# Optimization experiments

Measured on AMD Instinct MI355X. Metric: run time of the kernel, lower is better.

Reference implementation:

```python
import jax, jax.numpy as jnp
import numpy as np

B, N = 16, 4096
CH = 64          # channel
S = 1024         # groups (FPS samples)
K = 32           # kneighbors
D = 2 * CH       # aggregation width (in == out, residual-safe)
EPS_STD = 1e-5
BN_EPS = 1e-5
SLOPE = 0.01


def setup_inputs() -> dict:
    key = jax.random.key(0)
    ks = jax.random.split(key, 8)
    return {
        "xyz": jax.random.normal(ks[0], (B, N, 3), jnp.float32),
        "points": jax.random.normal(ks[1], (B, N, CH), jnp.float32),
        # LocalGrouper affine (use_xyz=False -> width CH)
        "affine_alpha": jnp.ones((1, 1, 1, CH), jnp.float32),
        "affine_beta": jnp.zeros((1, 1, 1, CH), jnp.float32),
        # Local_Aggregation: conv1d(k=1) + BN, twice
        "w1": jax.random.normal(ks[2], (D, D), jnp.float32) / np.sqrt(D),
        "b1": jax.random.normal(ks[3], (D,), jnp.float32) * 0.01,
        "g1": jnp.ones((D,), jnp.float32),
        "be1": jnp.zeros((D,), jnp.float32),
        "w2": jax.random.normal(ks[4], (D, D), jnp.float32) / np.sqrt(D),
        "b2": jax.random.normal(ks[5], (D,), jnp.float32) * 0.01,
        "g2": jnp.ones((D,), jnp.float32),
        "be2": jnp.zeros((D,), jnp.float32),
    }


def _fps_single(xyz):
    # Furthest point sampling for one cloud [N,3] -> [S] int32 (starts at index 0, matching CUDA FPS)
    n = xyz.shape[0]

    def body(carry, _):
        min_d, last = carry
        d = jnp.sum((xyz - xyz[last]) ** 2, axis=-1)   # [N]
        min_d = jnp.minimum(min_d, d)
        nxt = jnp.argmax(min_d).astype(jnp.int32)
        return (min_d, nxt), nxt

    init = (jnp.full((n,), 1e10, xyz.dtype), jnp.int32(0))
    _, idx_rest = jax.lax.scan(body, init, None, length=S - 1)
    return jnp.concatenate([jnp.zeros((1,), jnp.int32), idx_rest])


def _knn_single(xyz, new_xyz):
    # squared dists [S,N]; K smallest via top_k on negated distances
    d = (jnp.sum(new_xyz ** 2, -1, keepdims=True)
         + jnp.sum(xyz ** 2, -1)[None, :]
         - 2.0 * new_xyz @ xyz.T)
    _, idx = jax.lax.top_k(-d, K)
    return idx  # [S,K]


def _bn(x, g, b):
    # BatchNorm1d in training mode: batch stats over (batch, length) dims of [M, C, K]
    m = jnp.mean(x, axis=(0, 2), keepdims=True)
    v = jnp.mean((x - m) ** 2, axis=(0, 2), keepdims=True)  # biased var, as torch BN
    return g[None, :, None] * (x - m) * jax.lax.rsqrt(v + BN_EPS) + b[None, :, None]


def reference(xyz, points, affine_alpha, affine_beta, w1, b1, g1, be1, w2, b2, g2, be2):
    # ---- LocalGrouper ----
    fps_idx = jax.vmap(_fps_single)(xyz)                              # [B,S]
    new_xyz = jnp.take_along_axis(xyz, fps_idx[..., None], axis=1)    # [B,S,3]
    new_pts = jnp.take_along_axis(points, fps_idx[..., None], axis=1) # [B,S,CH]
    idx = jax.vmap(_knn_single)(xyz, new_xyz)                         # [B,S,K]
    grouped = jax.vmap(lambda p, i: p[i])(points, idx)                # [B,S,K,CH]

    # normalize == 'center': mean over neighbors, std over whole per-batch tensor (unbiased, as torch.std)
    mean = jnp.mean(grouped, axis=2, keepdims=True)                   # [B,S,1,CH]
    diff = grouped - mean
    cnt = S * K * CH
    var = jnp.sum(diff.reshape(B, -1) ** 2, axis=-1) / (cnt - 1)      # [B]
    std = jnp.sqrt(var)[:, None, None, None]                          # [B,1,1,1]
    grouped = affine_alpha * (diff / (std + EPS_STD)) + affine_beta

    new_feature = jnp.concatenate(
        [grouped, jnp.broadcast_to(new_pts[:, :, None, :], (B, S, K, CH))], axis=-1
    )                                                                  # [B,S,K,2*CH]

    # ---- Local_Aggregation ----
    x = new_feature.transpose(0, 1, 3, 2).reshape(B * S, D, K)         # [BS, D, K]
    h = jnp.einsum('oc,mck->mok', w1, x) + b1[None, :, None]
    h = jax.nn.leaky_relu(_bn(h, g1, be1), SLOPE)
    h = jnp.einsum('oc,mck->mok', w2, h) + b2[None, :, None]
    h = jax.nn.leaky_relu(_bn(h, g2, be2) + x, SLOPE)
    pooled = jnp.max(h, axis=-1).reshape(B, S, D)                      # adaptive_max_pool1d(.,1)
    return (new_xyz, pooled)
```

## Files before the change

kernel.cpp:

```cpp
#include <hip/hip_runtime.h>

#define DI __device__ __forceinline__

typedef __attribute__((ext_vector_type(8))) short v8s;
typedef __attribute__((ext_vector_type(4))) short v4s;
typedef __attribute__((ext_vector_type(4))) float v4f;
typedef unsigned long long u64;

constexpr int BB = 16, NN = 4096, CH = 64, SS = 1024, KK = 32, DD = 128;
constexpr int LDW = 136;
constexpr int GPC = 2;
constexpr int GGRID = 512;

constexpr size_t OFF_FPSIDX = 0;
constexpr size_t OFF_KNN    = 65536;
constexpr size_t OFF_MEAN   = 2162688;
constexpr size_t OFF_VARB   = 6356992;
constexpr size_t OFF_BINS1  = 6361088;
constexpr size_t OFF_BINS2  = 6426624;
constexpr size_t OFF_RSTD   = 6492160;
constexpr size_t OFF_COEF1  = 6492224;
constexpr size_t OFF_COEF2  = 6493248;
constexpr size_t OFF_W1BF   = 6494272;
constexpr size_t OFF_W2BF   = 6527040;
constexpr size_t OFF_XYZT   = 6559808;
constexpr size_t MEMSET_OFF = OFF_VARB;
constexpr size_t MEMSET_LEN = 4096 + 65536 + 65536;

DI short f2bf(float f) {
  unsigned u = __float_as_uint(f);
  u = (u + 0x7fffu + ((u >> 16) & 1u)) >> 16;
  return (short)u;
}
DI float bf2f(short s) { return __uint_as_float(((unsigned)(unsigned short)s) << 16); }

__global__ void prep_kernel(const float* __restrict__ xyz, float* __restrict__ xyzT,
                            const float* __restrict__ w1, const float* __restrict__ w2,
                            short* __restrict__ w1b, short* __restrict__ w2b) {
  int bid = blockIdx.x;
  if (bid < 256) {
    int i = bid * 256 + threadIdx.x;
    int b = i >> 12, n = i & 4095;
    const float* s = xyz + (size_t)i * 3;
    float* d = xyzT + (size_t)b * 3 * NN + n;
    d[0] = s[0]; d[NN] = s[1]; d[2 * NN] = s[2];
  } else {
    int i = (bid - 256) * 256 + threadIdx.x;
    w1b[i] = f2bf(w1[i]);
    w2b[i] = f2bf(w2[i]);
  }
}

DI double tag12(double d, int tag) {
  u64 b = (u64)__double_as_longlong(d);
  b = (b & ~0xFFFull) | (u64)(unsigned)tag;
  return __longlong_as_double((long long)b);
}
template <int CTRL>
DI double dpp_fmax64(double x) {
  u64 b = (u64)__double_as_longlong(x);
  int lo = __builtin_amdgcn_update_dpp(0, (int)(unsigned)b, CTRL, 0xf, 0xf, true);
  int hi = __builtin_amdgcn_update_dpp(0, (int)(unsigned)(b >> 32), CTRL, 0xf, 0xf, true);
  double o = __longlong_as_double((long long)(((u64)(unsigned)hi << 32) | (unsigned)lo));
  return fmax(x, o);
}
DI double readlane_f64(double x, int l) {
  u64 b = (u64)__double_as_longlong(x);
  unsigned lo = (unsigned)__builtin_amdgcn_readlane((int)(unsigned)b, l);
  unsigned hi = (unsigned)__builtin_amdgcn_readlane((int)(unsigned)(b >> 32), l);
  return __longlong_as_double((long long)(((u64)hi << 32) | lo));
}

template <int N>
DI float dpp_ror_f(float v) {
  return __int_as_float(__builtin_amdgcn_update_dpp(0, __float_as_int(v), 0x120 + N, 0xf, 0xf, true));
}
DI float sum16(float v) {
  v += dpp_ror_f<1>(v);
  v += dpp_ror_f<2>(v);
  v += dpp_ror_f<4>(v);
  v += dpp_ror_f<8>(v);
  return v;
}
DI float max16(float v) {
  v = fmaxf(v, dpp_ror_f<1>(v));
  v = fmaxf(v, dpp_ror_f<2>(v));
  v = fmaxf(v, dpp_ror_f<4>(v));
  v = fmaxf(v, dpp_ror_f<8>(v));
  return v;
}

__global__ __launch_bounds__(512, 2) void fps_kernel(const float* __restrict__ xyzT,
                                                     int* __restrict__ fps_idx,
                                                     float* __restrict__ out_xyz) {
  int b = blockIdx.x, tid = threadIdx.x;
  int wave = tid >> 6, lane = tid & 63;
  const float* bx = xyzT + (size_t)b * 3 * NN;
  const float* by = bx + NN;
  const float* bz = bx + 2 * NN;
  __shared__ float4 s_xyzw[NN];
  __shared__ int s_fidx[SS];
  __shared__ double s_pd[2][8];

  double px64[8], py64[8], pz64[8], pp64[8], m64[8];
  int tagbase = 4095 - tid;
#pragma unroll
  for (int k = 0; k < 8; ++k) {
    int gi = k * 512 + tid;
    float x = bx[gi], y = by[gi], z = bz[gi];
    s_xyzw[gi] = make_float4(x, y, z, 0.f);
    px64[k] = (double)x; py64[k] = (double)y; pz64[k] = (double)z;
    pp64[k] = fma(px64[k], px64[k], fma(py64[k], py64[k], pz64[k] * pz64[k]));
    m64[k] = tag12(1e10, tagbase - k * 512);
  }
  if (tid == 0) s_fidx[0] = 0;
  __syncthreads();
  float4 c0 = s_xyzw[0];
  double cx = (double)c0.x, cy = (double)c0.y, cz = (double)c0.z;

  for (int j = 1; j < SS; ++j) {
    double cx2 = -2.0 * cx, cy2 = -2.0 * cy, cz2 = -2.0 * cz;
    double cc = fma(cx, cx, fma(cy, cy, cz * cz));
    double best;
#pragma unroll
    for (int k = 0; k < 8; ++k) {
      double d = fma(px64[k], cx2, fma(py64[k], cy2, fma(pz64[k], cz2, pp64[k] + cc)));
      d = fmax(d, 0.0);
      d = tag12(d, tagbase - k * 512);
      m64[k] = fmin(m64[k], d);
      best = (k == 0) ? m64[0] : fmax(best, m64[k]);
    }
    best = dpp_fmax64<0xB1>(best);
    best = dpp_fmax64<0x4E>(best);
    best = dpp_fmax64<0x141>(best);
    best = dpp_fmax64<0x140>(best);
    double r0 = readlane_f64(best, 0);
    double r1 = readlane_f64(best, 16);
    double r2 = readlane_f64(best, 32);
    double r3 = readlane_f64(best, 48);
    double bw = fmax(fmax(r0, r1), fmax(r2, r3));
    if (lane == 0) s_pd[j & 1][wave] = bw;
    __syncthreads();
    double bk = s_pd[j & 1][0];
#pragma unroll
    for (int w = 1; w < 8; ++w) bk = fmax(bk, s_pd[j & 1][w]);
    int fi = 4095 - (int)((u64)__double_as_longlong(bk) & 0xFFFull);
    float4 cw = s_xyzw[fi];
    cx = (double)cw.x; cy = (double)cw.y; cz = (double)cw.z;
    if (tid == 0) s_fidx[j] = fi;
  }
  __syncthreads();
  for (int t = tid; t < SS; t += 512) {
    int idx = s_fidx[t];
    fps_idx[b * SS + t] = idx;
    float4 p = s_xyzw[idx];
    out_xyz[((size_t)b * SS + t) * 3 + 0] = p.x;
    out_xyz[((size_t)b * SS + t) * 3 + 1] = p.y;
    out_xyz[((size_t)b * SS + t) * 3 + 2] = p.z;
  }
}

__global__ __launch_bounds__(256) void knn_kernel(const float* __restrict__ xyzT,
                                                  const int* __restrict__ fps_idx,
                                                  int* __restrict__ knn_idx) {
  int wave = threadIdx.x >> 6, lane = threadIdx.x & 63;
  int q = blockIdx.x * 4 + wave, b = q >> 10;
  const float* bx = xyzT + (size_t)b * 3 * NN;
  const float* by = bx + NN;
  const float* bz = bx + 2 * NN;
  int qi = fps_idx[q];
  float qx = bx[qi], qy = by[qi], qz = bz[qi];
  float d[64];
  float lmin = 1e30f;
#pragma unroll
  for (int j = 0; j < 64; ++j) {
    int n = j * 64 + lane;
    float dx = bx[n] - qx, dy = by[n] - qy, dz = bz[n] - qz;
    d[j] = fmaf(dx, dx, fmaf(dy, dy, dz * dz));
    lmin = fminf(lmin, d[j]);
  }
  unsigned lb = __float_as_uint(lmin);
  unsigned res = 0;
#pragma unroll
  for (int bit = 30; bit >= 0; --bit) {
    unsigned t = res | (1u << bit);
    int c = __popcll(__ballot(lb < t));
    res = (c < 32) ? t : res;
  }
  float tau = __uint_as_float(res) * 1.00001f + 1e-20f;

  __shared__ int ci[4][512];
  __shared__ u64 ck[4][512];
  int cnt = 0;
#pragma unroll
  for (int j = 0; j < 64; ++j) {
    bool pred = (d[j] <= tau);
    unsigned long long mask = __ballot(pred);
    if (pred) {
      int pos = cnt + __popcll(mask & ((1ull << lane) - 1ull));
      if (pos < 512) ci[wave][pos] = j * 64 + lane;
    }
    cnt += __popcll(mask);
  }
  if (cnt > 512) cnt = 512;
  double qx64 = (double)qx, qy64 = (double)qy, qz64 = (double)qz;
  for (int p = lane; p < cnt; p += 64) {
    int n = ci[wave][p];
    double dx = (double)bx[n] - qx64;
    double dy = (double)by[n] - qy64;
    double dz = (double)bz[n] - qz64;
    double d64 = fma(dx, dx, fma(dy, dy, dz * dz));
    ck[wave][p] = ((u64)__double_as_longlong(d64) & ~0xFFFull) | (u64)n;
  }
  for (int p = lane; p < cnt; p += 64) {
    u64 mykey = ck[wave][p];
    int rank = 0;
    int r = 0;
    for (; r + 4 <= cnt; r += 4) {
      u64 k0 = ck[wave][r + 0], k1 = ck[wave][r + 1];
      u64 k2 = ck[wave][r + 2], k3 = ck[wave][r + 3];
      rank += (k0 < mykey) + (k1 < mykey) + (k2 < mykey) + (k3 < mykey);
    }
    for (; r < cnt; ++r) rank += (ck[wave][r] < mykey) ? 1 : 0;
    if (rank < KK) knn_idx[(size_t)q * KK + rank] = (int)(mykey & 0xFFFull);
  }
}

__global__ __launch_bounds__(256) void meanvar_kernel(const float* __restrict__ points,
                                                      const int* __restrict__ kidx,
                                                      float* __restrict__ mean_out,
                                                      float* __restrict__ var_bins) {
  int wave = threadIdx.x >> 6, lane = threadIdx.x & 63;
  int xcd = blockIdx.x & 7, slot = blockIdx.x >> 3;
  int b = xcd + ((slot >> 8) << 3);
  int g = b * SS + (slot & 255) * 4 + wave;
  const float* pb = points + (size_t)b * NN * CH;
  const int* idx = kidx + (size_t)g * KK;
  float s1 = 0.f, s2 = 0.f;
#pragma unroll
  for (int k = 0; k < KK; ++k) {
    float x = pb[(size_t)idx[k] * CH + lane];
    s1 += x;
    s2 = fmaf(x, x, s2);
  }
  float m = s1 * (1.0f / 32.0f);
  mean_out[(size_t)g * CH + lane] = m;
  float part = s2 - s1 * m;
#pragma unroll
  for (int mm = 1; mm < 64; mm <<= 1) part += __shfl_xor(part, mm, 64);
  if (lane == 0) atomicAdd(&var_bins[b * 64 + (g & 63)], part);
}

__global__ void fin_std_kernel(const float* __restrict__ bins, float* __restrict__ rstd) {
  int t = threadIdx.x;
  if (t < BB) {
    float s = 0.f;
    for (int i = 0; i < 64; ++i) s += bins[t * 64 + i];
    float var = s / (float)(SS * KK * CH - 1);
    rstd[t] = 1.0f / (sqrtf(var) + 1e-5f);
  }
}

__global__ void fin_bn_kernel(const float* __restrict__ bins, const float* __restrict__ g,
                              const float* __restrict__ be, float* __restrict__ coef) {
  int o = threadIdx.x;
  float s = 0.f, qq = 0.f;
  for (int bin = 0; bin < 64; ++bin) {
    s += bins[(bin * 128 + o) * 2 + 0];
    qq += bins[(bin * 128 + o) * 2 + 1];
  }
  constexpr float invM = 1.0f / (float)(BB * SS * KK);
  float mean = s * invM;
  float var = qq * invM - mean * mean;
  if (var < 0.f) var = 0.f;
  float sc = g[o] / sqrtf(var + 1e-5f);
  coef[2 * o] = sc;
  coef[2 * o + 1] = be[o] - mean * sc;
}

template <int PASS>
__global__ __launch_bounds__(256, 2) void gemm_pass(
    const float* __restrict__ points, const int* __restrict__ kidx, const int* __restrict__ fidx,
    const float* __restrict__ mean, const float* __restrict__ rstd,
    const float* __restrict__ alpha, const float* __restrict__ beta,
    const short* __restrict__ w1bf, const short* __restrict__ w2bf,
    const float* __restrict__ coef1, const float* __restrict__ coef2,
    float* __restrict__ bins_out, float* __restrict__ out_pooled) {
  __shared__ short Xs[GPC * 32 * LDW];
  __shared__ short Ps[(PASS >= 1) ? (GPC * 32 * LDW) : 8];
  __shared__ float sMean[2][GPC][64];
  __shared__ float sAlpha[64], sBeta[64];
  __shared__ float sCoef1[256], sCoef2[256];
  __shared__ float bnS[128], bnQ[128];

  int tid = threadIdx.x;
  int wave = tid >> 6, lane = tid & 63;
  int q4 = lane >> 4, l15 = lane & 15;
  int ohalf = wave & 1, gsel = wave >> 1;

  v8s wf1[4][4];
  v8s wf2[4][4];
#pragma unroll
  for (int ot = 0; ot < 4; ++ot) {
    int row = ohalf * 64 + ot * 16 + l15;
#pragma unroll
    for (int cs = 0; cs < 4; ++cs) {
      wf1[ot][cs] = *(const v8s*)(w1bf + row * 128 + cs * 32 + q4 * 8);
      if constexpr (PASS >= 1) wf2[ot][cs] = *(const v8s*)(w2bf + row * 128 + cs * 32 + q4 * 8);
    }
  }
  if (tid < 64) { sAlpha[tid] = alpha[tid]; sBeta[tid] = beta[tid]; }
  if constexpr (PASS >= 1) sCoef1[tid] = coef1[tid];
  if constexpr (PASS == 2) sCoef2[tid] = coef2[tid];
  if constexpr (PASS <= 1) {
    if (tid < 128) { bnS[tid] = 0.f; bnQ[tid] = 0.f; }
  }

  int xcd = blockIdx.x & 7, slot = blockIdx.x >> 3;
  int sg = tid >> 7, sk = (tid >> 2) & 31, qr = tid & 3;
  int ch0 = (qr & 1) * 32;
  bool norm = (qr < 2);
  float rsA = rstd[xcd], rsB = rstd[xcd + 8];

  float svA[4][4] = {}, sqA[4][4] = {};

  float4 ldv[8];
  {
    int t = slot;
    int batch = xcd + ((t >> 9) << 3);
    int g0 = batch * SS + (t & 511) * GPC;
    int ggl = g0 + sg;
    int row = norm ? kidx[(size_t)ggl * KK + sk] : fidx[ggl];
    const float* src = points + (size_t)batch * NN * CH + (size_t)row * CH + ch0;
#pragma unroll
    for (int u = 0; u < 8; ++u) ldv[u] = *(const float4*)(src + u * 4);
    if (tid < 32) {
      int sg2 = tid >> 4, off = (tid & 15) << 2;
      float4 mv = *(const float4*)(mean + (size_t)(g0 + sg2) * CH + off);
      *(float4*)&sMean[0][sg2][off] = mv;
    }
  }
  __syncthreads();

  for (int it = 0; it < 16; ++it) {
    int t = slot + it * 64;
    int batch = xcd + ((t >> 9) << 3);
    int g0 = batch * SS + (t & 511) * GPC;
    int tn = (it < 15) ? t + 64 : t;
    int batch_n = xcd + ((tn >> 9) << 3);
    int g0_n = batch_n * SS + (tn & 511) * GPC;
    int ggl_n = g0_n + sg;
    int row_n = norm ? kidx[(size_t)ggl_n * KK + sk] : fidx[ggl_n];

    {
      float rs = (t >> 9) ? rsB : rsA;
      v8s pack[4];
#pragma unroll
      for (int u = 0; u < 8; ++u) {
        float4 vv = ldv[u];
        if (norm) {
          float4 mv = *(const float4*)&sMean[it & 1][sg][ch0 + u * 4];
          float4 av = *(const float4*)&sAlpha[ch0 + u * 4];
          float4 bv = *(const float4*)&sBeta[ch0 + u * 4];
          vv.x = fmaf((vv.x - mv.x) * rs, av.x, bv.x);
          vv.y = fmaf((vv.y - mv.y) * rs, av.y, bv.y);
          vv.z = fmaf((vv.z - mv.z) * rs, av.z, bv.z);
          vv.w = fmaf((vv.w - mv.w) * rs, av.w, bv.w);
        }
        pack[u >> 1][(u & 1) * 4 + 0] = f2bf(vv.x);
        pack[u >> 1][(u & 1) * 4 + 1] = f2bf(vv.y);
        pack[u >> 1][(u & 1) * 4 + 2] = f2bf(vv.z);
        pack[u >> 1][(u & 1) * 4 + 3] = f2bf(vv.w);
      }
      short* dst = &Xs[(sg * 32 + sk) * LDW + qr * 32];
#pragma unroll
      for (int p2 = 0; p2 < 4; ++p2) *(v8s*)(dst + p2 * 8) = pack[p2];
    }
    __syncthreads();

    v4f acc[4][2] = {};
#pragma unroll
    for (int cs = 0; cs < 4; ++cs) {
      v8s bfr[2];
#pragma unroll
      for (int kt = 0; kt < 2; ++kt)
        bfr[kt] = *(const v8s*)&Xs[(gsel * 32 + kt * 16 + l15) * LDW + cs * 32 + q4 * 8];
#pragma unroll
      for (int ot = 0; ot < 4; ++ot)
#pragma unroll
        for (int kt = 0; kt < 2; ++kt)
          acc[ot][kt] = __builtin_amdgcn_mfma_f32_16x16x32_bf16(wf1[ot][cs], bfr[kt], acc[ot][kt], 0, 0, 0);
    }

    float4 mpre;
    {
      const float* src = points + (size_t)batch_n * NN * CH + (size_t)row_n * CH + ch0;
#pragma unroll
      for (int u = 0; u < 8; ++u) ldv[u] = *(const float4*)(src + u * 4);
      if (tid < 32) {
        int sg2 = tid >> 4, off = (tid & 15) << 2;
        mpre = *(const float4*)(mean + (size_t)(g0_n + sg2) * CH + off);
      }
    }

    if constexpr (PASS == 0) {
#pragma unroll
      for (int ot = 0; ot < 4; ++ot)
#pragma unroll
        for (int r = 0; r < 4; ++r) {
          float a0 = acc[ot][0][r], a1 = acc[ot][1][r];
          svA[ot][r] += a0 + a1;
          sqA[ot][r] = fmaf(a0, a0, fmaf(a1, a1, sqA[ot][r]));
        }
    } else {
#pragma unroll
      for (int ot = 0; ot < 4; ++ot) {
        int o0 = ohalf * 64 + ot * 16 + q4 * 4;
#pragma unroll
        for (int kt = 0; kt < 2; ++kt) {
          v4s pk;
#pragma unroll
          for (int r = 0; r < 4; ++r) {
            float h = fmaf(acc[ot][kt][r], sCoef1[2 * (o0 + r)], sCoef1[2 * (o0 + r) + 1]);
            h = (h >= 0.f) ? h : 0.01f * h;
            pk[r] = f2bf(h);
          }
          *(v4s*)&Ps[(gsel * 32 + kt * 16 + l15) * LDW + o0] = pk;
        }
      }
      __syncthreads();

      v4f acc2[4][2] = {};
#pragma unroll
      for (int cs = 0; cs < 4; ++cs) {
        v8s pfr[2];
#pragma unroll
        for (int kt = 0; kt < 2; ++kt)
          pfr[kt] = *(const v8s*)&Ps[(gsel * 32 + kt * 16 + l15) * LDW + cs * 32 + q4 * 8];
#pragma unroll
        for (int ot = 0; ot < 4; ++ot)
#pragma unroll
          for (int kt = 0; kt < 2; ++kt)
            acc2[ot][kt] = __builtin_amdgcn_mfma_f32_16x16x32_bf16(wf2[ot][cs], pfr[kt], acc2[ot][kt], 0, 0, 0);
      }

      if constexpr (PASS == 1) {
#pragma unroll
        for (int ot = 0; ot < 4; ++ot)
#pragma unroll
          for (int r = 0; r < 4; ++r) {
            float a0 = acc2[ot][0][r], a1 = acc2[ot][1][r];
            svA[ot][r] += a0 + a1;
            sqA[ot][r] = fmaf(a0, a0, fmaf(a1, a1, sqA[ot][r]));
          }
      } else {
#pragma unroll
        for (int ot = 0; ot < 4; ++ot) {
          int o0 = ohalf * 64 + ot * 16 + q4 * 4;
          float mx[4] = {-1e30f, -1e30f, -1e30f, -1e30f};
#pragma unroll
          for (int kt = 0; kt < 2; ++kt) {
            v4s xv = *(const v4s*)&Xs[(gsel * 32 + kt * 16 + l15) * LDW + o0];
#pragma unroll
            for (int r = 0; r < 4; ++r) {
              float h = fmaf(acc2[ot][kt][r], sCoef2[2 * (o0 + r)], sCoef2[2 * (o0 + r) + 1]);
              float val = h + bf2f(xv[r]);
              val = (val >= 0.f) ? val : 0.01f * val;
              mx[r] = fmaxf(mx[r], val);
            }
          }
#pragma unroll
          for (int r = 0; r < 4; ++r) mx[r] = max16(mx[r]);
          if (l15 == 0) {
            float4 o4;
            o4.x = mx[0]; o4.y = mx[1]; o4.z = mx[2]; o4.w = mx[3];
            *(float4*)(out_pooled + (size_t)(g0 + gsel) * DD + o0) = o4;
          }
        }
      }
    }
    if (tid < 32) *(float4*)&sMean[(it + 1) & 1][tid >> 4][(tid & 15) << 2] = mpre;
    __syncthreads();
  }

  if constexpr (PASS <= 1) {
#pragma unroll
    for (int ot = 0; ot < 4; ++ot)
#pragma unroll
      for (int r = 0; r < 4; ++r) {
        float sv = sum16(svA[ot][r]);
        float sq = sum16(sqA[ot][r]);
        if (l15 == 0) {
          int o0 = ohalf * 64 + ot * 16 + q4 * 4;
          atomicAdd(&bnS[o0 + r], sv);
          atomicAdd(&bnQ[o0 + r], sq);
        }
      }
    __syncthreads();
    if (tid < 128) {
      float* bb = bins_out + (((blockIdx.x & 63) * 128 + tid) << 1);
      atomicAdd(bb, bnS[tid]);
      atomicAdd(bb + 1, bnQ[tid]);
    }
  }
}

extern "C" void kernel_launch(void* const* d_in, const int* in_sizes, int n_in,
                              void* d_out, int out_size, void* d_ws, size_t ws_size,
                              hipStream_t stream) {
  const float* xyz    = (const float*)d_in[0];
  const float* points = (const float*)d_in[1];
  const float* alpha  = (const float*)d_in[2];
  const float* beta   = (const float*)d_in[3];
  const float* w1     = (const float*)d_in[4];
  const float* g1     = (const float*)d_in[6];
  const float* be1    = (const float*)d_in[7];
  const float* w2     = (const float*)d_in[8];
  const float* g2     = (const float*)d_in[10];
  const float* be2    = (const float*)d_in[11];
  float* out = (float*)d_out;

  char* w = (char*)d_ws;
  int* fps_i   = (int*)(w + OFF_FPSIDX);
  int* knn_i   = (int*)(w + OFF_KNN);
  float* meanp = (float*)(w + OFF_MEAN);
  float* varb  = (float*)(w + OFF_VARB);
  float* bins1 = (float*)(w + OFF_BINS1);
  float* bins2 = (float*)(w + OFF_BINS2);
  float* rstdp = (float*)(w + OFF_RSTD);
  float* coef1 = (float*)(w + OFF_COEF1);
  float* coef2 = (float*)(w + OFF_COEF2);
  short* w1b   = (short*)(w + OFF_W1BF);
  short* w2b   = (short*)(w + OFF_W2BF);
  float* xyzT  = (float*)(w + OFF_XYZT);

  hipMemsetAsync(w + MEMSET_OFF, 0, MEMSET_LEN, stream);
  prep_kernel<<<320, 256, 0, stream>>>(xyz, xyzT, w1, w2, w1b, w2b);
  fps_kernel<<<BB, 512, 0, stream>>>(xyzT, fps_i, out);
  knn_kernel<<<(BB * SS) / 4, 256, 0, stream>>>(xyzT, fps_i, knn_i);
  meanvar_kernel<<<(BB * SS) / 4, 256, 0, stream>>>(points, knn_i, meanp, varb);
  fin_std_kernel<<<1, 64, 0, stream>>>(varb, rstdp);
  gemm_pass<0><<<GGRID, 256, 0, stream>>>(points, knn_i, fps_i, meanp, rstdp, alpha, beta,
                                          w1b, w2b, coef1, coef2, bins1, nullptr);
  fin_bn_kernel<<<1, 128, 0, stream>>>(bins1, g1, be1, coef1);
  gemm_pass<1><<<GGRID, 256, 0, stream>>>(points, knn_i, fps_i, meanp, rstdp, alpha, beta,
                                          w1b, w2b, coef1, coef2, bins2, nullptr);
  fin_bn_kernel<<<1, 128, 0, stream>>>(bins2, g2, be2, coef2);
  gemm_pass<2><<<GGRID, 256, 0, stream>>>(points, knn_i, fps_i, meanp, rstdp, alpha, beta,
                                          w1b, w2b, coef1, coef2, nullptr, out + (size_t)BB * SS * 3);
}
```

Baseline: 1.055 ms.

## Shrink FPS block to 4 waves, fuse mean/var into KNN, use packed bf16 converts

The FPS kernel now runs 256 threads, each holding 16 points, so the per-iteration cross-wave reduction covers 4 waves instead of 8. The clamp to zero on distances is dropped. The mean/variance kernel is merged into the KNN kernel, reusing the selected neighbor indices from shared memory and removing one launch plus a global reread of the indices. The GEMM passes use a packed bf16 conversion builtin instead of manual rounding. The cost is more registers per FPS thread and less parallelism within the serial FPS loop. The ci array is also reused in place, which could be unsafe if other lanes still read candidate entries when the writes happen.

```diff
diff --git a/kernel.cpp b/kernel.cpp
--- a/kernel.cpp
+++ b/kernel.cpp
@@ -34,6 +34,16 @@
 }
 DI float bf2f(short s) { return __uint_as_float(((unsigned)(unsigned short)s) << 16); }
 
+DI unsigned pkbf(float a, float b) {
+#if __has_builtin(__builtin_amdgcn_cvt_pk_bf16_f32)
+  typedef __attribute__((ext_vector_type(2))) __bf16 bf2_t;
+  bf2_t r = __builtin_amdgcn_cvt_pk_bf16_f32(a, b);
+  return *(unsigned*)&r;
+#else
+  return (unsigned)(unsigned short)f2bf(a) | ((unsigned)(unsigned short)f2bf(b) << 16);
+#endif
+}
+
 __global__ void prep_kernel(const float* __restrict__ xyz, float* __restrict__ xyzT,
                             const float* __restrict__ w1, const float* __restrict__ w2,
                             short* __restrict__ w1b, short* __restrict__ w2b) {
@@ -90,7 +100,7 @@
   return v;
 }
 
-__global__ __launch_bounds__(512, 2) void fps_kernel(const float* __restrict__ xyzT,
+__global__ __launch_bounds__(256, 1) void fps_kernel(const float* __restrict__ xyzT,
                                                      int* __restrict__ fps_idx,
                                                      float* __restrict__ out_xyz) {
   int b = blockIdx.x, tid = threadIdx.x;
@@ -100,18 +110,18 @@
   const float* bz = bx + 2 * NN;
   __shared__ float4 s_xyzw[NN];
   __shared__ int s_fidx[SS];
-  __shared__ double s_pd[2][8];
-
-  double px64[8], py64[8], pz64[8], pp64[8], m64[8];
+  __shared__ double s_pd[2][4];
+
+  double px64[16], py64[16], pz64[16], pp64[16], m64[16];
   int tagbase = 4095 - tid;
 #pragma unroll
-  for (int k = 0; k < 8; ++k) {
-    int gi = k * 512 + tid;
+  for (int k = 0; k < 16; ++k) {
+    int gi = k * 256 + tid;
     float x = bx[gi], y = by[gi], z = bz[gi];
     s_xyzw[gi] = make_float4(x, y, z, 0.f);
     px64[k] = (double)x; py64[k] = (double)y; pz64[k] = (double)z;
     pp64[k] = fma(px64[k], px64[k], fma(py64[k], py64[k], pz64[k] * pz64[k]));
-    m64[k] = tag12(1e10, tagbase - k * 512);
+    m64[k] = tag12(1e10, tagbase - k * 256);
   }
   if (tid == 0) s_fidx[0] = 0;
   __syncthreads();
@@ -123,10 +133,9 @@
     double cc = fma(cx, cx, fma(cy, cy, cz * cz));
     double best;
 #pragma unroll
-    for (int k = 0; k < 8; ++k) {
+    for (int k = 0; k < 16; ++k) {
       double d = fma(px64[k], cx2, fma(py64[k], cy2, fma(pz64[k], cz2, pp64[k] + cc)));
-      d = fmax(d, 0.0);
-      d = tag12(d, tagbase - k * 512);
+      d = tag12(d, tagbase - k * 256);
       m64[k] = fmin(m64[k], d);
       best = (k == 0) ? m64[0] : fmax(best, m64[k]);
     }
@@ -141,16 +150,15 @@
     double bw = fmax(fmax(r0, r1), fmax(r2, r3));
     if (lane == 0) s_pd[j & 1][wave] = bw;
     __syncthreads();
-    double bk = s_pd[j & 1][0];
-#pragma unroll
-    for (int w = 1; w < 8; ++w) bk = fmax(bk, s_pd[j & 1][w]);
+    double bk = fmax(fmax(s_pd[j & 1][0], s_pd[j & 1][1]),
+                     fmax(s_pd[j & 1][2], s_pd[j & 1][3]));
     int fi = 4095 - (int)((u64)__double_as_longlong(bk) & 0xFFFull);
     float4 cw = s_xyzw[fi];
     cx = (double)cw.x; cy = (double)cw.y; cz = (double)cw.z;
     if (tid == 0) s_fidx[j] = fi;
   }
   __syncthreads();
-  for (int t = tid; t < SS; t += 512) {
+  for (int t = tid; t < SS; t += 256) {
     int idx = s_fidx[t];
     fps_idx[b * SS + t] = idx;
     float4 p = s_xyzw[idx];
@@ -162,7 +170,10 @@
 
 __global__ __launch_bounds__(256) void knn_kernel(const float* __restrict__ xyzT,
                                                   const int* __restrict__ fps_idx,
-                                                  int* __restrict__ knn_idx) {
+                                                  int* __restrict__ knn_idx,
+                                                  const float* __restrict__ points,
+                                                  float* __restrict__ mean_out,
+                                                  float* __restrict__ var_bins) {
   int wave = threadIdx.x >> 6, lane = threadIdx.x & 63;
   int q = blockIdx.x * 4 + wave, b = q >> 10;
   const float* bx = xyzT + (size_t)b * 3 * NN;
@@ -222,33 +233,26 @@
       rank += (k0 < mykey) + (k1 < mykey) + (k2 < mykey) + (k3 < mykey);
     }
     for (; r < cnt; ++r) rank += (ck[wave][r] < mykey) ? 1 : 0;
-    if (rank < KK) knn_idx[(size_t)q * KK + rank] = (int)(mykey & 0xFFFull);
-  }
-}
-
-__global__ __launch_bounds__(256) void meanvar_kernel(const float* __restrict__ points,
-                                                      const int* __restrict__ kidx,
-                                                      float* __restrict__ mean_out,
-                                                      float* __restrict__ var_bins) {
-  int wave = threadIdx.x >> 6, lane = threadIdx.x & 63;
-  int xcd = blockIdx.x & 7, slot = blockIdx.x >> 3;
-  int b = xcd + ((slot >> 8) << 3);
-  int g = b * SS + (slot & 255) * 4 + wave;
+    if (rank < KK) {
+      int n = (int)(mykey & 0xFFFull);
+      knn_idx[(size_t)q * KK + rank] = n;
+      ci[wave][rank] = n;
+    }
+  }
   const float* pb = points + (size_t)b * NN * CH;
-  const int* idx = kidx + (size_t)g * KK;
   float s1 = 0.f, s2 = 0.f;
 #pragma unroll
   for (int k = 0; k < KK; ++k) {
-    float x = pb[(size_t)idx[k] * CH + lane];
+    float x = pb[(size_t)ci[wave][k] * CH + lane];
     s1 += x;
     s2 = fmaf(x, x, s2);
   }
   float m = s1 * (1.0f / 32.0f);
-  mean_out[(size_t)g * CH + lane] = m;
+  mean_out[(size_t)q * CH + lane] = m;
   float part = s2 - s1 * m;
 #pragma unroll
   for (int mm = 1; mm < 64; mm <<= 1) part += __shfl_xor(part, mm, 64);
-  if (lane == 0) atomicAdd(&var_bins[b * 64 + (g & 63)], part);
+  if (lane == 0) atomicAdd(&var_bins[b * 64 + (q & 63)], part);
 }
 
 __global__ void fin_std_kernel(const float* __restrict__ bins, float* __restrict__ rstd) {
@@ -354,7 +358,7 @@
 
     {
       float rs = (t >> 9) ? rsB : rsA;
-      v8s pack[4];
+      unsigned pks[16];
 #pragma unroll
       for (int u = 0; u < 8; ++u) {
         float4 vv = ldv[u];
@@ -367,14 +371,12 @@
           vv.z = fmaf((vv.z - mv.z) * rs, av.z, bv.z);
           vv.w = fmaf((vv.w - mv.w) * rs, av.w, bv.w);
         }
-        pack[u >> 1][(u & 1) * 4 + 0] = f2bf(vv.x);
-        pack[u >> 1][(u & 1) * 4 + 1] = f2bf(vv.y);
-        pack[u >> 1][(u & 1) * 4 + 2] = f2bf(vv.z);
-        pack[u >> 1][(u & 1) * 4 + 3] = f2bf(vv.w);
+        pks[2 * u + 0] = pkbf(vv.x, vv.y);
+        pks[2 * u + 1] = pkbf(vv.z, vv.w);
       }
       short* dst = &Xs[(sg * 32 + sk) * LDW + qr * 32];
 #pragma unroll
-      for (int p2 = 0; p2 < 4; ++p2) *(v8s*)(dst + p2 * 8) = pack[p2];
+      for (int p2 = 0; p2 < 4; ++p2) *(uint4*)(dst + p2 * 8) = ((uint4*)pks)[p2];
     }
     __syncthreads();
 
@@ -418,14 +420,14 @@
         int o0 = ohalf * 64 + ot * 16 + q4 * 4;
 #pragma unroll
         for (int kt = 0; kt < 2; ++kt) {
-          v4s pk;
+          float hv[4];
 #pragma unroll
           for (int r = 0; r < 4; ++r) {
             float h = fmaf(acc[ot][kt][r], sCoef1[2 * (o0 + r)], sCoef1[2 * (o0 + r) + 1]);
-            h = (h >= 0.f) ? h : 0.01f * h;
-            pk[r] = f2bf(h);
+            hv[r] = (h >= 0.f) ? h : 0.01f * h;
           }
-          *(v4s*)&Ps[(gsel * 32 + kt * 16 + l15) * LDW + o0] = pk;
+          *(uint2*)&Ps[(gsel * 32 + kt * 16 + l15) * LDW + o0] =
+              make_uint2(pkbf(hv[0], hv[1]), pkbf(hv[2], hv[3]));
         }
       }
       __syncthreads();
@@ -536,9 +538,8 @@
 
   hipMemsetAsync(w + MEMSET_OFF, 0, MEMSET_LEN, stream);
   prep_kernel<<<320, 256, 0, stream>>>(xyz, xyzT, w1, w2, w1b, w2b);
-  fps_kernel<<<BB, 512, 0, stream>>>(xyzT, fps_i, out);
-  knn_kernel<<<(BB * SS) / 4, 256, 0, stream>>>(xyzT, fps_i, knn_i);
-  meanvar_kernel<<<(BB * SS) / 4, 256, 0, stream>>>(points, knn_i, meanp, varb);
+  fps_kernel<<<BB, 256, 0, stream>>>(xyzT, fps_i, out);
+  knn_kernel<<<(BB * SS) / 4, 256, 0, stream>>>(xyzT, fps_i, knn_i, points, meanp, varb);
   fin_std_kernel<<<1, 64, 0, stream>>>(varb, rstdp);
   gemm_pass<0><<<GGRID, 256, 0, stream>>>(points, knn_i, fps_i, meanp, rstdp, alpha, beta,
                                           w1b, w2b, coef1, coef2, bins1, nullptr);
```

New measurement: 967.2 us. 1.09x faster.
